# Performance work log

Hardware: AMD Instinct MI355X
Metric: run time of the kernel (lower is better)

Reference implementation:

```python
import jax, jax.numpy as jnp
import numpy as np

N = 64    # state dim n
K = 8     # mixture components
H = 1024  # fhat hidden
B = 65536
LOG2PI = float(np.log(2.0 * np.pi))

def setup_inputs() -> dict:
    key = jax.random.key(0)
    ks = jax.random.split(key, 8)
    x = jax.random.normal(ks[0], (B, N), jnp.float32)
    y = jax.random.normal(ks[1], (B, 1, N), jnp.float32)
    W1 = jax.random.normal(ks[2], (N, H), jnp.float32) / np.sqrt(N)
    b1 = jnp.zeros((H,), jnp.float32)
    W2 = jax.random.normal(ks[3], (H, 2 * K * N), jnp.float32) / np.sqrt(H)
    b2 = jnp.zeros((2 * K * N,), jnp.float32)
    Wp1 = jax.random.normal(ks[4], (N, N), jnp.float32) / np.sqrt(N)
    bp1 = jnp.zeros((N,), jnp.float32)
    Wp2 = jax.random.normal(ks[5], (N, K), jnp.float32) / np.sqrt(N)
    bp2 = jnp.zeros((K,), jnp.float32)
    return {"x": x, "y": y, "W1": W1, "b1": b1, "W2": W2, "b2": b2,
            "Wp1": Wp1, "bp1": bp1, "Wp2": Wp2, "bp2": bp2}

def _mdn_view(t):
    # torch.stack(t.split(n, dim=1)).view(-1, k, n): raw reshape of [k,B,n] -> [B,k,n]
    return jnp.stack(jnp.split(t, K, axis=1)).reshape(-1, K, N)

def reference(x, y, W1, b1, W2, b2, Wp1, bp1, Wp2, bp2):
    # fhat: Linear -> ELU -> Linear
    fhatx = jax.nn.elu(x @ W1 + b1) @ W2 + b2          # [B, 2*K*N]
    mu_raw, var_raw = jnp.split(fhatx, 2, axis=-1)     # each [B, K*N]
    mu = _mdn_view(mu_raw)                             # [B, K, N]
    var = jnp.maximum(jnp.exp(_mdn_view(var_raw)), 1e-8)
    # pi network: log probs of OneHotCategorical
    logits = jax.nn.elu(x @ Wp1 + bp1) @ Wp2 + bp2     # [B, K]
    log_pi = jax.nn.log_softmax(logits, axis=-1)
    # diagonal-covariance MVN log_prob (closed form, O(n))
    d = y - mu                                         # [B, K, N]
    logp_y = -0.5 * (jnp.sum(d * d / var + jnp.log(var), axis=-1) + N * LOG2PI)
    loss = jax.scipy.special.logsumexp(log_pi + logp_y, axis=-1)  # [B]
    return -jnp.mean(loss)
```

## Files before the change

kernel.cpp:

```cpp
#include <hip/hip_runtime.h>
#include <math.h>

typedef __attribute__((ext_vector_type(8))) _Float16 half8;
typedef __attribute__((ext_vector_type(4))) _Float16 half4;
typedef __attribute__((ext_vector_type(4))) float f32x4;

#define B_TOT 65536
#define LOG2PI_F 1.8378770664093453f
#define HALF_N_LOG2PI (0.5f * 64.0f * LOG2PI_F)
#define LOG_1EM8 (-18.420680743952367f)

#define WS_W2S  0
#define WS_W1P  (2u*1024*1024)
#define WS_LPS  (4u*1024*1024)
#define WS_PART (6u*1024*1024)
#define WS_HP   (8u*1024*1024)

typedef __attribute__((address_space(3))) unsigned int lds_u32;
typedef const __attribute__((address_space(1))) unsigned int glb_u32;

__device__ __forceinline__ void gload16(const void* g, void* l) {
    __builtin_amdgcn_global_load_lds((glb_u32*)g, (lds_u32*)l, 16, 0, 0);
}

__device__ __forceinline__ float eluf(float v) {
    return v > 0.0f ? v : expm1f(v);
}

__global__ __launch_bounds__(256)
void pack_w1(const float* __restrict__ src, _Float16* __restrict__ dst)
{
    __shared__ float ts[64][65];
    const int t = threadIdx.x;
    const int n0 = blockIdx.y * 64;
    {
        int r = t >> 2, c4 = t & 3;
        for (int i = 0; i < 4; ++i) {
            int cc = i * 4 + c4;
            float4 v = *(const float4*)&src[(size_t)r * 1024 + n0 + cc * 4];
            ts[r][cc*4+0] = v.x; ts[r][cc*4+1] = v.y;
            ts[r][cc*4+2] = v.z; ts[r][cc*4+3] = v.w;
        }
    }
    __syncthreads();
    {
        int n = t >> 2;
        for (int i = 0; i < 4; ++i) {
            int k = (i * 4 + (t & 3)) * 4;
            half4 h;
            h.x = (_Float16)ts[k+0][n];
            h.y = (_Float16)ts[k+1][n];
            h.z = (_Float16)ts[k+2][n];
            h.w = (_Float16)ts[k+3][n];
            size_t off = (size_t)(k >> 5) * 32768 + (size_t)(n0 + n) * 32 + (k & 31);
            *(half4*)&dst[off] = h;
        }
    }
}

__global__ __launch_bounds__(256)
void pack_w2s(const float* __restrict__ src, _Float16* __restrict__ dst)
{
    __shared__ float ts[64][65];
    const int t = threadIdx.x;
    const int k0 = blockIdx.x * 64, n0 = blockIdx.y * 64;
    {
        int r = t >> 2, c4 = t & 3;
        for (int i = 0; i < 4; ++i) {
            int cc = i * 4 + c4;
            float4 v = *(const float4*)&src[(size_t)(k0 + r) * 1024 + n0 + cc * 4];
            ts[r][cc*4+0] = v.x; ts[r][cc*4+1] = v.y;
            ts[r][cc*4+2] = v.z; ts[r][cc*4+3] = v.w;
        }
    }
    __syncthreads();
    {
        int n = t >> 2;
        int ng = n0 + n;
        for (int i = 0; i < 4; ++i) {
            int kl = (i * 4 + (t & 3)) * 4;
            int k = k0 + kl;
            half4 h;
            h.x = (_Float16)ts[kl+0][n];
            h.y = (_Float16)ts[kl+1][n];
            h.z = (_Float16)ts[kl+2][n];
            h.w = (_Float16)ts[kl+3][n];
            int kk = k & 31;
            int slot = ((kk >> 3) ^ ((ng >> 1) & 3));
            size_t off = (size_t)(k >> 5) * 32768 + (size_t)ng * 32 + (slot << 3) + (kk & 7);
            *(half4*)&dst[off] = h;
        }
    }
}

__global__ __launch_bounds__(1024)
void k1_h(const float* __restrict__ x, const _Float16* __restrict__ W1P,
          const float* __restrict__ b1, _Float16* __restrict__ hp)
{
    __shared__ __align__(16) _Float16 xs[32 * 64];
    __shared__ __align__(16) _Float16 stage[32 * 32 * 32];
    const int t = threadIdx.x, q = blockIdx.x;
    const int w = t >> 6, l = t & 63, g = l >> 4, l15 = l & 15;

    if (t < 512) {
        const float4* x4 = (const float4*)x;
        int r = t >> 4, c = t & 15;
        float4 v = x4[(size_t)(q * 32 + r) * 16 + c];
        float vv[4] = {v.x, v.y, v.z, v.w};
        #pragma unroll
        for (int i = 0; i < 4; ++i) {
            int col = c * 4 + i;
            xs[r * 64 + (col ^ ((r & 7) << 3))] = (_Float16)vv[i];
        }
    }
    __syncthreads();

    f32x4 acc[2][4];
    #pragma unroll
    for (int ct = 0; ct < 4; ++ct) {
        float bv = b1[w * 64 + ct * 16 + l15];
        acc[0][ct] = (f32x4){bv, bv, bv, bv};
        acc[1][ct] = (f32x4){bv, bv, bv, bv};
    }
    #pragma unroll
    for (int k0 = 0; k0 < 64; k0 += 32) {
        half8 bF[4];
        #pragma unroll
        for (int ct = 0; ct < 4; ++ct) {
            size_t off = (size_t)(k0 >> 5) * 32768 + (size_t)(w * 64 + ct * 16 + l15) * 32 + 8 * g;
            bF[ct] = *(const half8*)&W1P[off];
        }
        half8 aF[2];
        #pragma unroll
        for (int rt = 0; rt < 2; ++rt) {
            int row = rt * 16 + l15;
            aF[rt] = *(const half8*)&xs[row * 64 + ((k0 + 8 * g) ^ ((row & 7) << 3))];
        }
        #pragma unroll
        for (int ct = 0; ct < 4; ++ct)
            #pragma unroll
            for (int rt = 0; rt < 2; ++rt)
                acc[rt][ct] = __builtin_amdgcn_mfma_f32_16x16x32_f16(aF[rt], bF[ct], acc[rt][ct], 0, 0, 0);
    }
    #pragma unroll
    for (int rt = 0; rt < 2; ++rt)
        #pragma unroll
        for (int ct = 0; ct < 4; ++ct)
            #pragma unroll
            for (int rg = 0; rg < 4; ++rg) {
                float v = eluf(acc[rt][ct][rg]);
                int rowl = rt * 16 + 4 * g + rg;
                int col = w * 64 + ct * 16 + l15;
                int kk = col & 31;
                int slot = (kk >> 3) ^ ((rowl >> 1) & 3);
                stage[((col >> 5) * 32 + rowl) * 32 + (slot << 3) + (kk & 7)] = (_Float16)v;
            }
    __syncthreads();
    #pragma unroll
    for (int i = 0; i < 4; ++i) {
        int flat8 = (i * 1024 + t) * 8;
        int kt = flat8 >> 10;
        int rem = flat8 & 1023;
        *(half8*)&hp[(size_t)kt * 2097152 + (size_t)q * 1024 + rem] = *(const half8*)&stage[flat8];
    }
}

__global__ __launch_bounds__(512)
void k2_gemm2(const _Float16* __restrict__ hp, const _Float16* __restrict__ W2S,
              const float* __restrict__ b2, const float* __restrict__ y,
              float* __restrict__ lps)
{
    __shared__ __align__(16) _Float16 Ab[2][4096];
    __shared__ __align__(16) _Float16 Bb[2][8192];
    __shared__ float lpp[128][2][2];

    const int t = threadIdx.x;
    const int bid = blockIdx.x;
    const int logical = (bid & 7) * 256 + (bid >> 3);
    const int RT = logical >> 2;
    const int j  = logical & 3;
    const int w = t >> 6, l = t & 63, g = l >> 4, l15 = l & 15;
    const int wr = w >> 2, wc = w & 3;

    int bn[4];
    bn[0] = (wc >> 1) * 64 + (wc & 1) * 32 + l15;
    bn[1] = bn[0] + 16;
    bn[2] = bn[0] + 128;
    bn[3] = bn[1] + 128;

    f32x4 acc[4][4];
    #pragma unroll
    for (int fc = 0; fc < 4; ++fc) {
        int colg = (fc < 2) ? (j * 128 + bn[fc]) : (512 + j * 128 + bn[fc] - 128);
        float bv = b2[colg];
        #pragma unroll
        for (int fr = 0; fr < 4; ++fr) acc[fr][fc] = (f32x4){bv, bv, bv, bv};
    }

    const char* hpb  = (const char*)hp;
    const char* w2sb = (const char*)W2S;
    const int lane16 = l * 16;

    {
        size_t ga = ((size_t)0 * 65536 + (size_t)RT * 128) * 64 + w * 1024 + lane16;
        gload16(hpb + ga, (char*)&Ab[0][0] + w * 1024);
        size_t gb0 = ((size_t)0 * 1024 + j * 128) * 64 + w * 1024 + lane16;
        gload16(w2sb + gb0, (char*)&Bb[0][0] + w * 1024);
        size_t gb1 = ((size_t)0 * 1024 + 512 + j * 128) * 64 + w * 1024 + lane16;
        gload16(w2sb + gb1, (char*)&Bb[0][0] + 8192 + w * 1024);
    }
    __syncthreads();

    for (int kt = 0; kt < 32; ++kt) {
        int cur = kt & 1;
        if (kt < 31) {
            int nx = cur ^ 1;
            size_t ga = ((size_t)(kt + 1) * 65536 + (size_t)RT * 128) * 64 + w * 1024 + lane16;
            gload16(hpb + ga, (char*)&Ab[nx][0] + w * 1024);
            size_t gb0 = ((size_t)(kt + 1) * 1024 + j * 128) * 64 + w * 1024 + lane16;
            gload16(w2sb + gb0, (char*)&Bb[nx][0] + w * 1024);
            size_t gb1 = ((size_t)(kt + 1) * 1024 + 512 + j * 128) * 64 + w * 1024 + lane16;
            gload16(w2sb + gb1, (char*)&Bb[nx][0] + 8192 + w * 1024);
        }
        half8 aF[4], bF[4];
        #pragma unroll
        for (int fr = 0; fr < 4; ++fr) {
            int r = wr * 64 + fr * 16 + l15;
            aF[fr] = *(const half8*)((const char*)&Ab[cur][0] + r * 64 + ((g ^ ((r >> 1) & 3)) << 4));
        }
        #pragma unroll
        for (int fc = 0; fc < 4; ++fc) {
            int n = bn[fc];
            bF[fc] = *(const half8*)((const char*)&Bb[cur][0] + n * 64 + ((g ^ ((n >> 1) & 3)) << 4));
        }
        #pragma unroll
        for (int fc = 0; fc < 4; ++fc)
            #pragma unroll
            for (int fr = 0; fr < 4; ++fr)
                acc[fr][fc] = __builtin_amdgcn_mfma_f32_16x16x32_f16(aF[fr], bF[fc], acc[fr][fc], 0, 0, 0);
        __syncthreads();
    }

    const int jj = j * 2 + (wc >> 1);
    float s[4][4];
    #pragma unroll
    for (int fr = 0; fr < 4; ++fr)
        #pragma unroll
        for (int rg = 0; rg < 4; ++rg) s[fr][rg] = 0.0f;

    #pragma unroll
    for (int fc = 0; fc < 2; ++fc) {
        int n = (wc & 1) * 32 + fc * 16 + l15;
        #pragma unroll
        for (int fr = 0; fr < 4; ++fr)
            #pragma unroll
            for (int rg = 0; rg < 4; ++rg) {
                int grow = RT * 128 + wr * 64 + fr * 16 + 4 * g + rg;
                int bp = (grow >> 3) + jj * 8192;
                float yv = y[(size_t)bp * 64 + n];
                float mu = acc[fr][fc][rg];
                float vr = acc[fr][fc + 2][rg];
                float vre = fmaxf(vr, LOG_1EM8);
                float iv = (vr >= LOG_1EM8) ? expf(-vr) : 1e8f;
                float d = yv - mu;
                s[fr][rg] += fmaf(d * d, iv, vre);
            }
    }
    #pragma unroll
    for (int fr = 0; fr < 4; ++fr)
        #pragma unroll
        for (int rg = 0; rg < 4; ++rg) {
            float v = s[fr][rg];
            v += __shfl_xor(v, 1); v += __shfl_xor(v, 2);
            v += __shfl_xor(v, 4); v += __shfl_xor(v, 8);
            s[fr][rg] = v;
        }
    if (l15 == 0) {
        #pragma unroll
        for (int fr = 0; fr < 4; ++fr)
            #pragma unroll
            for (int rg = 0; rg < 4; ++rg)
                lpp[wr * 64 + fr * 16 + 4 * g + rg][wc >> 1][wc & 1] = s[fr][rg];
    }
    __syncthreads();
    if (t < 256) {
        int row_l = t >> 1, m = t & 1;
        float lp = -0.5f * (lpp[row_l][m][0] + lpp[row_l][m][1]) - HALF_N_LOG2PI;
        int grow = RT * 128 + row_l;
        int bp = (grow >> 3) + (j * 2 + m) * 8192;
        lps[(size_t)bp * 8 + (grow & 7)] = lp;
    }
}

__global__ __launch_bounds__(256)
void k3_pi(const float* __restrict__ x, const float* __restrict__ Wp1,
           const float* __restrict__ bp1, const float* __restrict__ Wp2,
           const float* __restrict__ bp2, const float* __restrict__ lps,
           float* __restrict__ partials)
{
    __shared__ float xsl[256][65];
    __shared__ float w1s[64][65];
    __shared__ float w2s[64][8];
    __shared__ float wsum[4];
    const int t = threadIdx.x;
    const int b0 = blockIdx.x * 256;

    {
        const float4* x4 = (const float4*)x;
        for (int i = 0; i < 16; ++i) {
            int idx = t + i * 256;
            int r = idx >> 4, c = idx & 15;
            float4 v = x4[(size_t)(b0 + r) * 16 + c];
            xsl[r][c*4+0] = v.x; xsl[r][c*4+1] = v.y;
            xsl[r][c*4+2] = v.z; xsl[r][c*4+3] = v.w;
        }
        for (int i = 0; i < 16; ++i) {
            int idx = t + i * 256;
            int r = idx >> 6, c = idx & 63;
            w1s[r][c] = Wp1[r * 64 + c];
        }
        ((float*)w2s)[t] = Wp2[t];
        ((float*)w2s)[t + 256] = Wp2[t + 256];
    }
    __syncthreads();

    float hid[64];
    #pragma unroll
    for (int c = 0; c < 64; ++c) hid[c] = bp1[c];
    for (int n = 0; n < 64; ++n) {
        float xv = xsl[t][n];
        #pragma unroll
        for (int c = 0; c < 64; ++c) hid[c] = fmaf(xv, w1s[n][c], hid[c]);
    }
    float lg[8];
    #pragma unroll
    for (int k = 0; k < 8; ++k) lg[k] = bp2[k];
    #pragma unroll
    for (int c = 0; c < 64; ++c) {
        float e = eluf(hid[c]);
        #pragma unroll
        for (int k = 0; k < 8; ++k) lg[k] = fmaf(e, w2s[c][k], lg[k]);
    }
    float4 lpa = *(const float4*)&lps[(size_t)(b0 + t) * 8];
    float4 lpb = *(const float4*)&lps[(size_t)(b0 + t) * 8 + 4];
    float lp[8] = {lpa.x, lpa.y, lpa.z, lpa.w, lpb.x, lpb.y, lpb.z, lpb.w};

    float m1 = lg[0];
    #pragma unroll
    for (int k = 1; k < 8; ++k) m1 = fmaxf(m1, lg[k]);
    float den = 0.0f;
    #pragma unroll
    for (int k = 0; k < 8; ++k) den += expf(lg[k] - m1);
    float lden = logf(den);

    float v0 = lg[0] - m1 - lden + lp[0];
    float m2 = v0;
    float vv[8]; vv[0] = v0;
    #pragma unroll
    for (int k = 1; k < 8; ++k) {
        vv[k] = lg[k] - m1 - lden + lp[k];
        m2 = fmaxf(m2, vv[k]);
    }
    float s2 = 0.0f;
    #pragma unroll
    for (int k = 0; k < 8; ++k) s2 += expf(vv[k] - m2);
    float loss = m2 + logf(s2);

    float ssum = loss;
    ssum += __shfl_xor(ssum, 1);  ssum += __shfl_xor(ssum, 2);
    ssum += __shfl_xor(ssum, 4);  ssum += __shfl_xor(ssum, 8);
    ssum += __shfl_xor(ssum, 16); ssum += __shfl_xor(ssum, 32);
    if ((t & 63) == 0) wsum[t >> 6] = ssum;
    __syncthreads();
    if (t == 0) partials[blockIdx.x] = wsum[0] + wsum[1] + wsum[2] + wsum[3];
}

__global__ void k4_reduce(const float* __restrict__ partials, float* __restrict__ out)
{
    __shared__ double red[256];
    int t = threadIdx.x;
    red[t] = (double)partials[t];
    __syncthreads();
    for (int s = 128; s > 0; s >>= 1) {
        if (t < s) red[t] += red[t + s];
        __syncthreads();
    }
    if (t == 0) out[0] = (float)(-red[0] / (double)B_TOT);
}

extern "C" void kernel_launch(void* const* d_in, const int* in_sizes, int n_in,
                              void* d_out, int out_size, void* d_ws, size_t ws_size,
                              hipStream_t stream)
{
    const float* x   = (const float*)d_in[0];
    const float* y   = (const float*)d_in[1];
    const float* W1  = (const float*)d_in[2];
    const float* b1  = (const float*)d_in[3];
    const float* W2  = (const float*)d_in[4];
    const float* b2  = (const float*)d_in[5];
    const float* Wp1 = (const float*)d_in[6];
    const float* bp1 = (const float*)d_in[7];
    const float* Wp2 = (const float*)d_in[8];
    const float* bp2 = (const float*)d_in[9];

    char* ws = (char*)d_ws;
    _Float16* W2S = (_Float16*)(ws + WS_W2S);
    _Float16* W1P = (_Float16*)(ws + WS_W1P);
    float* lps      = (float*)(ws + WS_LPS);
    float* partials = (float*)(ws + WS_PART);
    _Float16* hp    = (_Float16*)(ws + WS_HP);

    pack_w2s<<<dim3(16, 16), 256, 0, stream>>>(W2, W2S);
    pack_w1<<<dim3(1, 16), 256, 0, stream>>>(W1, W1P);
    k1_h<<<2048, 1024, 0, stream>>>(x, W1P, b1, hp);
    k2_gemm2<<<2048, 512, 0, stream>>>(hp, W2S, b2, y, lps);
    k3_pi<<<256, 256, 0, stream>>>(x, Wp1, bp1, Wp2, bp2, lps, partials);
    k4_reduce<<<1, 256, 0, stream>>>(partials, (float*)d_out);
}
```

Baseline: 261.4 us.

## Swap MFMA operands in k1 to store hidden activations directly without LDS staging

The first GEMM kernel now puts W1 in the A operand and x in the B operand, so each lane's accumulator holds four consecutive hidden columns for one row. Those values can be written straight to the swizzled global layout as half4 stores, with no LDS stage buffer and no second barrier. The block also shrinks from 1024 to 512 threads, each doing twice as many MFMA tiles. This cuts LDS traffic and a synchronisation but uses narrower 8-byte global stores and more accumulator registers per thread.

```diff
diff --git a/kernel.cpp b/kernel.cpp
--- a/kernel.cpp
+++ b/kernel.cpp
@@ -93,16 +93,15 @@
     }
 }
 
-__global__ __launch_bounds__(1024)
+__global__ __launch_bounds__(512)
 void k1_h(const float* __restrict__ x, const _Float16* __restrict__ W1P,
           const float* __restrict__ b1, _Float16* __restrict__ hp)
 {
     __shared__ __align__(16) _Float16 xs[32 * 64];
-    __shared__ __align__(16) _Float16 stage[32 * 32 * 32];
     const int t = threadIdx.x, q = blockIdx.x;
     const int w = t >> 6, l = t & 63, g = l >> 4, l15 = l & 15;
 
-    if (t < 512) {
+    {
         const float4* x4 = (const float4*)x;
         int r = t >> 4, c = t & 15;
         float4 v = x4[(size_t)(q * 32 + r) * 16 + c];
@@ -115,53 +114,47 @@
     }
     __syncthreads();
 
-    f32x4 acc[2][4];
-    #pragma unroll
-    for (int ct = 0; ct < 4; ++ct) {
-        float bv = b1[w * 64 + ct * 16 + l15];
-        acc[0][ct] = (f32x4){bv, bv, bv, bv};
-        acc[1][ct] = (f32x4){bv, bv, bv, bv};
+    f32x4 acc[8][2];
+    const float4* b1_4 = (const float4*)b1;
+    #pragma unroll
+    for (int nf = 0; nf < 8; ++nf) {
+        float4 bv = b1_4[(w * 128 + nf * 16 + 4 * g) >> 2];
+        acc[nf][0] = (f32x4){bv.x, bv.y, bv.z, bv.w};
+        acc[nf][1] = acc[nf][0];
     }
     #pragma unroll
     for (int k0 = 0; k0 < 64; k0 += 32) {
-        half8 bF[4];
-        #pragma unroll
-        for (int ct = 0; ct < 4; ++ct) {
-            size_t off = (size_t)(k0 >> 5) * 32768 + (size_t)(w * 64 + ct * 16 + l15) * 32 + 8 * g;
-            bF[ct] = *(const half8*)&W1P[off];
-        }
-        half8 aF[2];
-        #pragma unroll
-        for (int rt = 0; rt < 2; ++rt) {
-            int row = rt * 16 + l15;
-            aF[rt] = *(const half8*)&xs[row * 64 + ((k0 + 8 * g) ^ ((row & 7) << 3))];
-        }
-        #pragma unroll
-        for (int ct = 0; ct < 4; ++ct)
+        half8 bx[2];
+        #pragma unroll
+        for (int rf = 0; rf < 2; ++rf) {
+            int row = rf * 16 + l15;
+            bx[rf] = *(const half8*)&xs[row * 64 + ((k0 + 8 * g) ^ ((row & 7) << 3))];
+        }
+        #pragma unroll
+        for (int nf = 0; nf < 8; ++nf) {
+            size_t off = (size_t)(k0 >> 5) * 32768 + (size_t)(w * 128 + nf * 16 + l15) * 32 + 8 * g;
+            half8 aw = *(const half8*)&W1P[off];
             #pragma unroll
-            for (int rt = 0; rt < 2; ++rt)
-                acc[rt][ct] = __builtin_amdgcn_mfma_f32_16x16x32_f16(aF[rt], bF[ct], acc[rt][ct], 0, 0, 0);
-    }
-    #pragma unroll
-    for (int rt = 0; rt < 2; ++rt)
-        #pragma unroll
-        for (int ct = 0; ct < 4; ++ct)
-            #pragma unroll
-            for (int rg = 0; rg < 4; ++rg) {
-                float v = eluf(acc[rt][ct][rg]);
-                int rowl = rt * 16 + 4 * g + rg;
-                int col = w * 64 + ct * 16 + l15;
-                int kk = col & 31;
-                int slot = (kk >> 3) ^ ((rowl >> 1) & 3);
-                stage[((col >> 5) * 32 + rowl) * 32 + (slot << 3) + (kk & 7)] = (_Float16)v;
-            }
-    __syncthreads();
-    #pragma unroll
-    for (int i = 0; i < 4; ++i) {
-        int flat8 = (i * 1024 + t) * 8;
-        int kt = flat8 >> 10;
-        int rem = flat8 & 1023;
-        *(half8*)&hp[(size_t)kt * 2097152 + (size_t)q * 1024 + rem] = *(const half8*)&stage[flat8];
+            for (int rf = 0; rf < 2; ++rf)
+                acc[nf][rf] = __builtin_amdgcn_mfma_f32_16x16x32_f16(aw, bx[rf], acc[nf][rf], 0, 0, 0);
+        }
+    }
+    #pragma unroll
+    for (int nf = 0; nf < 8; ++nf) {
+        int kt = w * 4 + (nf >> 1);
+        int kkhi = (nf & 1) * 2 + (g >> 1);
+        int kklo = 4 * (g & 1);
+        #pragma unroll
+        for (int rf = 0; rf < 2; ++rf) {
+            int grow = q * 32 + rf * 16 + l15;
+            int slot = kkhi ^ ((grow >> 1) & 3);
+            half4 h4;
+            h4.x = (_Float16)eluf(acc[nf][rf][0]);
+            h4.y = (_Float16)eluf(acc[nf][rf][1]);
+            h4.z = (_Float16)eluf(acc[nf][rf][2]);
+            h4.w = (_Float16)eluf(acc[nf][rf][3]);
+            *(half4*)&hp[(size_t)kt * 2097152 + (size_t)grow * 32 + slot * 8 + kklo] = h4;
+        }
     }
 }
 
@@ -412,7 +405,7 @@
 
     pack_w2s<<<dim3(16, 16), 256, 0, stream>>>(W2, W2S);
     pack_w1<<<dim3(1, 16), 256, 0, stream>>>(W1, W1P);
-    k1_h<<<2048, 1024, 0, stream>>>(x, W1P, b1, hp);
+    k1_h<<<2048, 512, 0, stream>>>(x, W1P, b1, hp);
     k2_gemm2<<<2048, 512, 0, stream>>>(hp, W2S, b2, y, lps);
     k3_pi<<<256, 256, 0, stream>>>(x, Wp1, bp1, Wp2, bp2, lps, partials);
     k4_reduce<<<1, 256, 0, stream>>>(partials, (float*)d_out);
```

After: 248.6 us. -4.9%, faster.
